# Performance work log

Hardware: AMD Instinct MI355X
Metric: run time of the kernel (lower is better)

## Reference

```python
import jax, jax.numpy as jnp
import numpy as np

K2 = 4.0 / 3.0; K4 = 4.10451; K5 = 19.08857; K6 = 254.5553148552
KN = 7.5; WF = 6.0; GA = 3.0; GC = 2.0
BOHR = 0.5291772105638411; HARTREE = 27.211386024367243
C2BOHR = 1.0 / BOHR; C2EV = 0.5 * HARTREE
N_ATOMS = 50000; N_NEIGH = 48; ZMAX = 87; NREF = 7; NFREQ = 23; KCN = 7


def _sp_inv(x):
    # softplus_inverse
    return jnp.float32(np.log(np.expm1(x)))


def setup_inputs() -> dict:
    key = jax.random.key(0)
    ks = jax.random.split(key, 24)
    P = N_ATOMS * N_NEIGH
    u = lambda k, shp, lo, hi: jax.random.uniform(k, shp, jnp.float32, lo, hi)
    Z = jax.random.randint(ks[0], (N_ATOMS,), 0, ZMAX)
    idx_i = jnp.repeat(jnp.arange(N_ATOMS), N_NEIGH)  # center index per pair
    idx_j = jax.random.randint(ks[1], (P,), 0, N_ATOMS)
    r_ij = u(ks[2], (P,), 1.5, 6.0)  # Angstrom
    qa = 0.05 * jax.random.normal(ks[3], (N_ATOMS,), jnp.float32)
    return dict(
        Z=Z, idx_i=idx_i, idx_j=idx_j, r_ij=r_ij, qa=qa,
        s6_raw=_sp_inv(1.0), s8_raw=_sp_inv(1.61679827),
        a1_raw=_sp_inv(0.44959224), a2_raw=_sp_inv(3.35743605),
        scaleq_raw=_sp_inv(1.0),
        refsys=jax.random.randint(ks[4], (ZMAX, NREF), 0, ZMAX),
        zeff=u(ks[5], (ZMAX,), 1.0, 10.0),
        refh=u(ks[6], (ZMAX, NREF), 0.0, 0.3),
        sscale=u(ks[7], (ZMAX,), 0.5, 1.5),
        secaiw=u(ks[8], (ZMAX, NFREQ), 0.0, 1.0),
        gam=u(ks[9], (ZMAX,), 0.05, 0.5),
        ascale=u(ks[10], (ZMAX, NREF), 0.5, 1.5),
        alphaiw=u(ks[11], (ZMAX, NREF, NFREQ), 0.0, 5.0),
        hcount=u(ks[12], (ZMAX, NREF), 0.0, 2.0),
        casimir_polder_weights=u(ks[13], (NFREQ,), 0.0, 0.5),
        rcov=u(ks[14], (ZMAX,), 0.6, 2.5),
        en=u(ks[15], (ZMAX,), 0.5, 4.0),
        ncount_mask=(u(ks[16], (ZMAX, NREF, KCN), 0.0, 1.0) < 0.6).astype(jnp.float32),
        ncount_weight=u(ks[17], (ZMAX, NREF, KCN), 0.5, 2.0),
        cn=u(ks[18], (ZMAX, NREF, KCN), 0.0, 6.0),
        fixgweights=(lambda g: g / jnp.sum(g, -1, keepdims=True))(u(ks[19], (ZMAX, NREF), 0.1, 1.0)),
        refq=u(ks[20], (ZMAX, NREF), -0.2, 0.2),
        sqrt_r4r2=u(ks[21], (ZMAX,), 1.0, 4.0),
    )


def compute_refc6(scaleq, refsys, zeff, refh, sscale, secaiw, gam, ascale, alphaiw, hcount, cpw):
    iz = zeff[refsys]                                   # [Z, nref]
    qref = iz
    qmod = iz + refh * scaleq
    qmod_ = jnp.where(qmod > 1e-8, qmod, 1.0)
    zeta = jnp.where(qmod > 1e-8,
                     jnp.exp(GA * (1.0 - jnp.exp(gam[refsys] * GC * (1.0 - qref / qmod_)))),
                     np.exp(GA).astype(np.float32))
    asec = sscale[refsys][..., None] * secaiw[refsys] * zeta[..., None]  # [Z,nref,nfreq]
    alpha = jnp.maximum(ascale[..., None] * (alphaiw - hcount[..., None] * asec), 0.0)
    return (3.0 / np.pi) * jnp.einsum('iax,jbx,x->ijab', alpha, alpha, cpw)  # [Z,Z,nref,nref]


def reference(Z, idx_i, idx_j, r_ij, qa, s6_raw, s8_raw, a1_raw, a2_raw, scaleq_raw,
              refsys, zeff, refh, sscale, secaiw, gam, ascale, alphaiw, hcount,
              casimir_polder_weights, rcov, en, ncount_mask, ncount_weight, cn,
              fixgweights, refq, sqrt_r4r2):
    n_atoms = qa.shape[0]
    scaleq = jax.nn.softplus(scaleq_raw)
    # refc6 is computed under no_grad in the original module
    refc6 = jax.lax.stop_gradient(compute_refc6(scaleq, refsys, zeff, refh, sscale,
                                                secaiw, gam, ascale, alphaiw, hcount,
                                                casimir_polder_weights))
    r = r_ij * C2BOHR
    Zi = Z[idx_i]; Zj = Z[idx_j]
    # coordination-number contribution per pair, scattered to centers
    rco = K2 * (rcov[Zi] + rcov[Zj])
    den = K4 * jnp.exp(-(jnp.abs(en[Zi] - en[Zj]) + K5) ** 2 / K6)
    tmp = den * 0.5 * (1.0 + jax.lax.erf(-KN * (r - rco) / rco))
    covcn = jax.ops.segment_sum(tmp, idx_i, num_segments=n_atoms)
    # gaussian reference-CN weights [n_atoms, nref]
    gweights = jnp.sum(ncount_mask[Z] * jnp.exp(-WF * ncount_weight[Z] * (covcn[:, None, None] - cn[Z]) ** 2), -1)
    norm = jnp.sum(gweights, -1, keepdims=True)
    gweights = jnp.where(norm > 1e-8, gweights / jnp.where(norm > 1e-8, norm, 1.0), fixgweights[Z])
    # charge scaling zeta [n_atoms, nref]
    iz = zeff[Z][:, None]
    qref = iz + refq[Z] * scaleq
    qmod = iz + qa[:, None]
    qmod_ = jnp.where(qmod > 1e-8, qmod, 1.0)
    zeta = jnp.where(qmod > 1e-8,
                     jnp.exp(GA * (1.0 - jnp.exp(gam[Z][:, None] * GC * (1.0 - qref / qmod_)))),
                     np.exp(GA).astype(np.float32)) * gweights
    zetai = zeta[idx_i]; zetaj = zeta[idx_j]            # [P, nref]
    refc6ij = refc6[Zi, Zj]                             # [P, nref, nref]
    c6ij = jnp.einsum('pab,pa,pb->p', refc6ij, zetai, zetaj)
    r4r2ij = np.float32(np.sqrt(3.0)) * sqrt_r4r2[Zi] * sqrt_r4r2[Zj]
    a1 = jax.nn.softplus(a1_raw); a2 = jax.nn.softplus(a2_raw)
    r0 = a1 * r4r2ij + a2
    oor6 = 1.0 / (r ** 6 + r0 ** 6)
    oor8 = 1.0 / (r ** 8 + r0 ** 8)
    s6 = jax.nn.softplus(s6_raw); s8 = jax.nn.softplus(s8_raw)
    edisp = -c6ij * (s6 * oor6 + s8 * r4r2ij ** 2 * oor8) * C2EV
    eatom = jax.ops.segment_sum(edisp, idx_i, num_segments=n_atoms)
    zeros = jnp.zeros((n_atoms,), r_ij.dtype)  # compute_atomic_quantities=False
    return (eatom, zeros, zeros)
```

## Files before the change

kernel.cpp:

```cpp
#include <hip/hip_runtime.h>
#include <hip/hip_fp16.h>
#include <math.h>

#define NATOMS 50000
#define NNEIGH 48
#define ZMAXV 87
#define NREFV 7
#define NFREQV 23
#define KCNV 7
#define XPAD 24
#define XPADH 32
#define APB 8
#define TPB 192
#define PPB (APB * NNEIGH)

#define C2BOHR 1.8897261258369282f
#define C2EV 13.605693012183622f
#define K2C 1.33333333333333333f
#define K4C 4.10451f
#define K5C 19.08857f
#define K6INV (1.0f / 254.5553148552f)
#define KNC 7.5f
#define EXP_GA 20.085536923187668f
#define QRT3 1.3160740129524924f

__device__ __forceinline__ float sp(float x) { return log1pf(expf(x)); }

__device__ __forceinline__ float fast_erf(float x) {
    float ax = fabsf(x);
    float t = 1.0f / fmaf(0.3275911f, ax, 1.0f);
    float poly = t * fmaf(t, fmaf(t, fmaf(t, fmaf(t, 1.061405429f, -1.453152027f),
                                          1.421413741f), -0.284496736f), 0.254829592f);
    float y = 1.0f - poly * __expf(-ax * ax);
    return copysignf(y, x);
}

__global__ __launch_bounds__(256) void k_setup(
    const int* __restrict__ Z, const int* __restrict__ refsys,
    const float* __restrict__ zeff, const float* __restrict__ refh,
    const float* __restrict__ sscale, const float* __restrict__ secaiw,
    const float* __restrict__ gam, const float* __restrict__ ascale,
    const float* __restrict__ alphaiw, const float* __restrict__ hcount,
    const float* __restrict__ rcov, const float* __restrict__ en,
    const float* __restrict__ s6r, const float* __restrict__ s8r,
    const float* __restrict__ a1r, const float* __restrict__ a2r,
    const float* __restrict__ sqr,
    float* __restrict__ scal_out, float* __restrict__ alpha_out,
    float2* __restrict__ re2_out, float* __restrict__ zero_out)
{
    int e = blockIdx.x * 256 + threadIdx.x;
    if (e == 0) {
        scal_out[0] = sp(s6r[0]);
        scal_out[1] = sp(s8r[0]);
        scal_out[2] = sp(a1r[0]);
        scal_out[3] = sp(a2r[0]);
        scal_out[4] = sp(sqr[0]);
    }
    if (e < 2 * NATOMS) zero_out[e] = 0.0f;
    if (e < NATOMS) {
        int z = Z[e];
        re2_out[e] = make_float2(rcov[z], en[z]);
    }
    if (e < ZMAXV * NREFV * XPAD) {
        int x = e % XPAD;
        int za = e / XPAD;
        float v = 0.0f;
        if (x < NFREQV) {
            float scaleq = sp(sqr[0]);
            int rs = refsys[za];
            float iz = zeff[rs];
            float qmod = iz + refh[za] * scaleq;
            float zeta = (qmod > 1e-8f)
                ? __expf(3.0f * (1.0f - __expf(gam[rs] * 2.0f * (1.0f - iz / qmod))))
                : EXP_GA;
            float asec = sscale[rs] * secaiw[rs * NFREQV + x] * zeta;
            v = fmaxf(ascale[za] * (alphaiw[za * NFREQV + x] - hcount[za] * asec), 0.0f);
        }
        alpha_out[e] = v;
    }
}

__global__ __launch_bounds__(TPB) void k_atoms(
    const int* __restrict__ Z, const int* __restrict__ idx_j,
    const float* __restrict__ r_ij, const float* __restrict__ qa,
    const float* __restrict__ scal, const float* __restrict__ zeff,
    const float* __restrict__ gam, const float2* __restrict__ re2,
    const float* __restrict__ nmask, const float* __restrict__ nweight,
    const float* __restrict__ cn, const float* __restrict__ fixg,
    const float* __restrict__ refq, const float* __restrict__ cpw,
    const float* __restrict__ alpha_tab, const float* __restrict__ sr4r2,
    __half2* __restrict__ A_out2)
{
    __shared__ float sh[TPB];
    __shared__ float covcn[APB];
    __shared__ float gwl[APB][NREFV];
    __shared__ float ztl[APB][NREFV];
    const int t = threadIdx.x;
    const int a0 = blockIdx.x * APB;
    const int al = t / 24;
    const int kk = t - al * 24;

    {
        int p0 = blockIdx.x * PPB + al * NNEIGH + kk;
        int p1 = p0 + 24;
        int j0 = __builtin_nontemporal_load(idx_j + p0);
        int j1 = __builtin_nontemporal_load(idx_j + p1);
        float rr0 = __builtin_nontemporal_load(r_ij + p0);
        float rr1 = __builtin_nontemporal_load(r_ij + p1);
        float2 rej0 = re2[j0];
        float2 rej1 = re2[j1];
        float2 rei = re2[a0 + al];

        float r0 = rr0 * C2BOHR;
        float rco0 = K2C * (rei.x + rej0.x);
        float d0 = fabsf(rei.y - rej0.y) + K5C;
        float den0 = K4C * __expf(-d0 * d0 * K6INV);
        float t0 = den0 * 0.5f * (1.0f + fast_erf(-KNC * (r0 - rco0) / rco0));

        float r1 = rr1 * C2BOHR;
        float rco1 = K2C * (rei.x + rej1.x);
        float d1 = fabsf(rei.y - rej1.y) + K5C;
        float den1 = K4C * __expf(-d1 * d1 * K6INV);
        float t1 = den1 * 0.5f * (1.0f + fast_erf(-KNC * (r1 - rco1) / rco1));

        sh[t] = t0 + t1;
    }
    __syncthreads();
    if (t < APB) {
        float s = 0.0f;
        for (int k = 0; k < 24; k++) s += sh[t * 24 + k];
        covcn[t] = s;
    }
    __syncthreads();

    if (t < APB * NREFV) {
        int a_l = t / NREFV, a = t % NREFV;
        int zl = Z[a0 + a_l];
        float cc = covcn[a_l];
        const float* mB = nmask + (zl * NREFV + a) * KCNV;
        const float* wB = nweight + (zl * NREFV + a) * KCNV;
        const float* cB = cn + (zl * NREFV + a) * KCNV;
        float g = 0.0f;
        for (int k = 0; k < KCNV; k++) {
            float dc = cc - cB[k];
            g += mB[k] * __expf(-6.0f * wB[k] * dc * dc);
        }
        gwl[a_l][a] = g;
    }
    __syncthreads();

    if (t < APB * NREFV) {
        int a_l = t / NREFV, a = t % NREFV;
        int zl = Z[a0 + a_l];
        float norm = 0.0f;
        for (int b = 0; b < NREFV; b++) norm += gwl[a_l][b];
        float w = (norm > 1e-8f) ? (gwl[a_l][a] / norm) : fixg[zl * NREFV + a];
        float scaleq = scal[4];
        float iz = zeff[zl];
        float qref = iz + refq[zl * NREFV + a] * scaleq;
        float qmod = iz + qa[a0 + a_l];
        float zeta = (qmod > 1e-8f)
            ? __expf(3.0f * (1.0f - __expf(gam[zl] * 2.0f * (1.0f - qref / qmod))))
            : EXP_GA;
        ztl[a_l][a] = zeta * w;
    }
    __syncthreads();

    if (t < APB * (XPADH / 2)) {
        int a_l = t >> 4, xh = t & 15;
        int x0 = 2 * xh, x1 = 2 * xh + 1;
        int zl = Z[a0 + a_l];
        float v0 = 0.0f, v1 = 0.0f;
        if (x0 < NFREQV) {
            float s = 0.0f;
            #pragma unroll
            for (int a = 0; a < NREFV; a++)
                s += ztl[a_l][a] * alpha_tab[(zl * NREFV + a) * XPAD + x0];
            v0 = s * sqrtf(cpw[x0] * 0.9549296585513721f);
        }
        if (x1 < NFREQV) {
            float s = 0.0f;
            #pragma unroll
            for (int a = 0; a < NREFV; a++)
                s += ztl[a_l][a] * alpha_tab[(zl * NREFV + a) * XPAD + x1];
            v1 = s * sqrtf(cpw[x1] * 0.9549296585513721f);
        } else if (x1 == NFREQV) {
            v1 = QRT3 * sr4r2[zl];
        }
        A_out2[(size_t)(a0 + a_l) * (XPADH / 2) + xh] = __floats2half2_rn(v0, v1);
    }
}

__global__ __launch_bounds__(TPB) void k_pairs(
    const int* __restrict__ idx_j, const float* __restrict__ r_ij,
    const float* __restrict__ scal, const __half* __restrict__ Ah,
    float* __restrict__ eatom)
{
    __shared__ float sh[TPB];
    __shared__ float Ai[APB][NFREQV];
    __shared__ float Asi[APB];
    const int t = threadIdx.x;
    const int a0 = blockIdx.x * APB;
    const int al = t / 24;
    const int kk = t - al * 24;

    {
        float v = __half2float(Ah[(size_t)(a0 + al) * XPADH + kk]);
        if (kk < NFREQV) Ai[al][kk] = v;
        else Asi[al] = v;
    }
    __syncthreads();

    const float s6 = scal[0], s8 = scal[1], a1 = scal[2], a2 = scal[3];

    int p0 = blockIdx.x * PPB + al * NNEIGH + kk;
    int p1 = p0 + 24;
    int j0 = __builtin_nontemporal_load(idx_j + p0);
    int j1 = __builtin_nontemporal_load(idx_j + p1);
    float rr0 = __builtin_nontemporal_load(r_ij + p0);
    float rr1 = __builtin_nontemporal_load(r_ij + p1);

    const float4* P0 = (const float4*)(Ah + (size_t)j0 * XPADH);
    const float4* P1 = (const float4*)(Ah + (size_t)j1 * XPADH);
    float4 u0 = P0[0], u1 = P0[1], u2 = P0[2];
    float4 w0 = P1[0], w1 = P1[1], w2 = P1[2];

    float c60 = 0.0f, c61 = 0.0f, sj0 = 0.0f, sj1 = 0.0f;
    {
        const __half2* a2p[3] = { (const __half2*)&u0, (const __half2*)&u1, (const __half2*)&u2 };
        const __half2* b2p[3] = { (const __half2*)&w0, (const __half2*)&w1, (const __half2*)&w2 };
        #pragma unroll
        for (int seg = 0; seg < 3; seg++) {
            #pragma unroll
            for (int k = 0; k < 4; k++) {
                int x = seg * 8 + 2 * k;
                float2 fa = __half22float2(a2p[seg][k]);
                float2 fb = __half22float2(b2p[seg][k]);
                if (x < NFREQV) { c60 += fa.x * Ai[al][x]; c61 += fb.x * Ai[al][x]; }
                if (x + 1 < NFREQV) { c60 += fa.y * Ai[al][x + 1]; c61 += fb.y * Ai[al][x + 1]; }
                else if (x + 1 == NFREQV) { sj0 = fa.y; sj1 = fb.y; }
            }
        }
    }

    float e0, e1;
    {
        float r = rr0 * C2BOHR;
        float r4r2 = Asi[al] * sj0;
        float r0v = a1 * r4r2 + a2;
        float r2 = r * r, r4 = r2 * r2, r6 = r4 * r2, r8 = r4 * r4;
        float p2 = r0v * r0v, p4 = p2 * p2, p6 = p4 * p2, p8 = p4 * p4;
        e0 = -c60 * (s6 / (r6 + p6) + s8 * r4r2 * r4r2 / (r8 + p8)) * C2EV;
    }
    {
        float r = rr1 * C2BOHR;
        float r4r2 = Asi[al] * sj1;
        float r0v = a1 * r4r2 + a2;
        float r2 = r * r, r4 = r2 * r2, r6 = r4 * r2, r8 = r4 * r4;
        float p2 = r0v * r0v, p4 = p2 * p2, p6 = p4 * p2, p8 = p4 * p4;
        e1 = -c61 * (s6 / (r6 + p6) + s8 * r4r2 * r4r2 / (r8 + p8)) * C2EV;
    }

    sh[t] = e0 + e1;
    __syncthreads();
    if (t < APB) {
        float s = 0.0f;
        for (int k = 0; k < 24; k++) s += sh[t * 24 + k];
        eatom[a0 + t] = s;
    }
}

extern "C" void kernel_launch(void* const* d_in, const int* in_sizes, int n_in,
                              void* d_out, int out_size, void* d_ws, size_t ws_size,
                              hipStream_t stream)
{
    const int*   Z       = (const int*)  d_in[0];
    const int*   idx_j   = (const int*)  d_in[2];
    const float* r_ij    = (const float*)d_in[3];
    const float* qa      = (const float*)d_in[4];
    const float* s6r     = (const float*)d_in[5];
    const float* s8r     = (const float*)d_in[6];
    const float* a1r     = (const float*)d_in[7];
    const float* a2r     = (const float*)d_in[8];
    const float* sqraw   = (const float*)d_in[9];
    const int*   refsys  = (const int*)  d_in[10];
    const float* zeff    = (const float*)d_in[11];
    const float* refh    = (const float*)d_in[12];
    const float* sscale  = (const float*)d_in[13];
    const float* secaiw  = (const float*)d_in[14];
    const float* gam     = (const float*)d_in[15];
    const float* ascale  = (const float*)d_in[16];
    const float* alphaiw = (const float*)d_in[17];
    const float* hcount  = (const float*)d_in[18];
    const float* cpw     = (const float*)d_in[19];
    const float* rcov    = (const float*)d_in[20];
    const float* en      = (const float*)d_in[21];
    const float* nmask   = (const float*)d_in[22];
    const float* nweight = (const float*)d_in[23];
    const float* cn      = (const float*)d_in[24];
    const float* fixg    = (const float*)d_in[25];
    const float* refq    = (const float*)d_in[26];
    const float* sr4r2   = (const float*)d_in[27];

    char* wsb = (char*)d_ws;
    float*  scal  = (float*)(wsb);
    float*  alpha = (float*)(wsb + 64);
    float2* re2   = (float2*)(wsb + 58528);
    __half* Ah    = (__half*)(wsb + 458752);

    float* eatom = (float*)d_out;
    float* zeros = eatom + NATOMS;

    k_setup<<<391, 256, 0, stream>>>(Z, refsys, zeff, refh, sscale, secaiw, gam,
                                     ascale, alphaiw, hcount, rcov, en,
                                     s6r, s8r, a1r, a2r, sqraw,
                                     scal, alpha, re2, zeros);
    k_atoms<<<NATOMS / APB, TPB, 0, stream>>>(
        Z, idx_j, r_ij, qa, scal, zeff, gam, re2,
        nmask, nweight, cn, fixg, refq, cpw, alpha, sr4r2, (__half2*)Ah);
    k_pairs<<<NATOMS / APB, TPB, 0, stream>>>(
        idx_j, r_ij, scal, Ah, eatom);
}
```

Before: 186.5 us.

## Split each pair's gathered row across four lanes with shuffle reduction in k_pairs

Measured after the change: 174.0 us. -6.7%, faster.

```diff
diff --git a/kernel.cpp b/kernel.cpp
--- a/kernel.cpp
+++ b/kernel.cpp
@@ -13,6 +13,8 @@
 #define APB 8
 #define TPB 192
 #define PPB (APB * NNEIGH)
+#define P_APB 4
+#define P_TPB 256
 
 #define C2BOHR 1.8897261258369282f
 #define C2EV 13.605693012183622f
@@ -103,10 +105,10 @@
     {
         int p0 = blockIdx.x * PPB + al * NNEIGH + kk;
         int p1 = p0 + 24;
-        int j0 = __builtin_nontemporal_load(idx_j + p0);
-        int j1 = __builtin_nontemporal_load(idx_j + p1);
-        float rr0 = __builtin_nontemporal_load(r_ij + p0);
-        float rr1 = __builtin_nontemporal_load(r_ij + p1);
+        int j0 = idx_j[p0];
+        int j1 = idx_j[p1];
+        float rr0 = r_ij[p0];
+        float rr1 = r_ij[p1];
         float2 rej0 = re2[j0];
         float2 rej1 = re2[j1];
         float2 rei = re2[a0 + al];
@@ -191,82 +193,74 @@
     }
 }
 
-__global__ __launch_bounds__(TPB) void k_pairs(
+__global__ __launch_bounds__(P_TPB) void k_pairs(
     const int* __restrict__ idx_j, const float* __restrict__ r_ij,
     const float* __restrict__ scal, const __half* __restrict__ Ah,
     float* __restrict__ eatom)
 {
-    __shared__ float sh[TPB];
-    __shared__ float Ai[APB][NFREQV];
-    __shared__ float Asi[APB];
+    __shared__ float sh[P_APB * NNEIGH];
+    __shared__ float AiP[P_APB][32];
+    __shared__ float Asi[P_APB];
     const int t = threadIdx.x;
-    const int a0 = blockIdx.x * APB;
-    const int al = t / 24;
-    const int kk = t - al * 24;
-
-    {
-        float v = __half2float(Ah[(size_t)(a0 + al) * XPADH + kk]);
-        if (kk < NFREQV) Ai[al][kk] = v;
-        else Asi[al] = v;
+    const int a0 = blockIdx.x * P_APB;
+
+    if (t < P_APB * 32) {
+        int al = t >> 5, x = t & 31;
+        float v = __half2float(Ah[(size_t)(a0 + al) * XPADH + x]);
+        AiP[al][x] = (x < NFREQV) ? v : 0.0f;
+        if (x == NFREQV) Asi[al] = v;
     }
     __syncthreads();
 
     const float s6 = scal[0], s8 = scal[1], a1 = scal[2], a2 = scal[3];
-
-    int p0 = blockIdx.x * PPB + al * NNEIGH + kk;
-    int p1 = p0 + 24;
-    int j0 = __builtin_nontemporal_load(idx_j + p0);
-    int j1 = __builtin_nontemporal_load(idx_j + p1);
-    float rr0 = __builtin_nontemporal_load(r_ij + p0);
-    float rr1 = __builtin_nontemporal_load(r_ij + p1);
-
-    const float4* P0 = (const float4*)(Ah + (size_t)j0 * XPADH);
-    const float4* P1 = (const float4*)(Ah + (size_t)j1 * XPADH);
-    float4 u0 = P0[0], u1 = P0[1], u2 = P0[2];
-    float4 w0 = P1[0], w1 = P1[1], w2 = P1[2];
-
-    float c60 = 0.0f, c61 = 0.0f, sj0 = 0.0f, sj1 = 0.0f;
-    {
-        const __half2* a2p[3] = { (const __half2*)&u0, (const __half2*)&u1, (const __half2*)&u2 };
-        const __half2* b2p[3] = { (const __half2*)&w0, (const __half2*)&w1, (const __half2*)&w2 };
+    const int q = t >> 2;
+    const int l = t & 3;
+    const int pb = blockIdx.x * (P_APB * NNEIGH);
+
+    int pl[3]; int jj[3]; float rr[3]; float4 ch[3];
+    #pragma unroll
+    for (int s = 0; s < 3; s++) {
+        pl[s] = q + 64 * s;
+        int p = pb + pl[s];
+        jj[s] = idx_j[p];
+        rr[s] = r_ij[p];
+    }
+    #pragma unroll
+    for (int s = 0; s < 3; s++)
+        ch[s] = ((const float4*)(Ah + (size_t)jj[s] * XPADH))[l];
+
+    #pragma unroll
+    for (int s = 0; s < 3; s++) {
+        int al = pl[s] / NNEIGH;
+        const __half2* h2 = (const __half2*)&ch[s];
+        float part = 0.0f, sjp = 0.0f;
+        int xb = l * 8;
         #pragma unroll
-        for (int seg = 0; seg < 3; seg++) {
-            #pragma unroll
-            for (int k = 0; k < 4; k++) {
-                int x = seg * 8 + 2 * k;
-                float2 fa = __half22float2(a2p[seg][k]);
-                float2 fb = __half22float2(b2p[seg][k]);
-                if (x < NFREQV) { c60 += fa.x * Ai[al][x]; c61 += fb.x * Ai[al][x]; }
-                if (x + 1 < NFREQV) { c60 += fa.y * Ai[al][x + 1]; c61 += fb.y * Ai[al][x + 1]; }
-                else if (x + 1 == NFREQV) { sj0 = fa.y; sj1 = fb.y; }
-            }
-        }
-    }
-
-    float e0, e1;
-    {
-        float r = rr0 * C2BOHR;
-        float r4r2 = Asi[al] * sj0;
+        for (int k = 0; k < 4; k++) {
+            float2 f = __half22float2(h2[k]);
+            int x0 = xb + 2 * k, x1 = x0 + 1;
+            part += f.x * AiP[al][x0];
+            part += f.y * AiP[al][x1];
+            if (x1 == NFREQV) sjp = f.y;
+        }
+        part += __shfl_xor(part, 1, 64);
+        part += __shfl_xor(part, 2, 64);
+        sjp  += __shfl_xor(sjp, 1, 64);
+        sjp  += __shfl_xor(sjp, 2, 64);
+
+        float r = rr[s] * C2BOHR;
+        float r4r2 = Asi[al] * sjp;
         float r0v = a1 * r4r2 + a2;
         float r2 = r * r, r4 = r2 * r2, r6 = r4 * r2, r8 = r4 * r4;
         float p2 = r0v * r0v, p4 = p2 * p2, p6 = p4 * p2, p8 = p4 * p4;
-        e0 = -c60 * (s6 / (r6 + p6) + s8 * r4r2 * r4r2 / (r8 + p8)) * C2EV;
-    }
-    {
-        float r = rr1 * C2BOHR;
-        float r4r2 = Asi[al] * sj1;
-        float r0v = a1 * r4r2 + a2;
-        float r2 = r * r, r4 = r2 * r2, r6 = r4 * r2, r8 = r4 * r4;
-        float p2 = r0v * r0v, p4 = p2 * p2, p6 = p4 * p2, p8 = p4 * p4;
-        e1 = -c61 * (s6 / (r6 + p6) + s8 * r4r2 * r4r2 / (r8 + p8)) * C2EV;
-    }
-
-    sh[t] = e0 + e1;
-    __syncthreads();
-    if (t < APB) {
-        float s = 0.0f;
-        for (int k = 0; k < 24; k++) s += sh[t * 24 + k];
-        eatom[a0 + t] = s;
+        float e = -part * (s6 / (r6 + p6) + s8 * r4r2 * r4r2 / (r8 + p8)) * C2EV;
+        if (l == 0) sh[pl[s]] = e;
+    }
+    __syncthreads();
+    if (t < P_APB) {
+        float ssum = 0.0f;
+        for (int k = 0; k < NNEIGH; k++) ssum += sh[t * NNEIGH + k];
+        eatom[a0 + t] = ssum;
     }
 }
 
@@ -318,6 +312,6 @@
     k_atoms<<<NATOMS / APB, TPB, 0, stream>>>(
         Z, idx_j, r_ij, qa, scal, zeff, gam, re2,
         nmask, nweight, cn, fixg, refq, cpw, alpha, sr4r2, (__half2*)Ah);
-    k_pairs<<<NATOMS / APB, TPB, 0, stream>>>(
+    k_pairs<<<NATOMS / P_APB, P_TPB, 0, stream>>>(
         idx_j, r_ij, scal, Ah, eatom);
 }
```
